# Kernel optimization log

Hardware: AMD Instinct MI355X
Metric: run time of the kernel (lower is better)

Reference implementation:

```python
import math
import jax, jax.numpy as jnp
import numpy as np

B, C, T = 8, 512, 4096
DK = max(C // 8, 2)          # 64
SCALE = math.sqrt(DK)        # 8.0
GAMMA = 1.0                  # source inits gamma=0 (identity); use 1.0 to exercise the attention path
EPS = 1e-12


def _l2_normalize(v):
    return v / (jnp.linalg.norm(v) + EPS)


def setup_inputs() -> dict:
    key = jax.random.key(0)
    ks = jax.random.split(key, 5)
    return {
        "x": jax.random.normal(ks[0], (B, C, T), jnp.float32),
        "Wq": jax.random.normal(ks[1], (DK, C), jnp.float32) * 0.05,
        "Wk": jax.random.normal(ks[2], (DK, C), jnp.float32) * 0.05,
        "Wv": jax.random.normal(ks[3], (C, C), jnp.float32) * 0.05,
        "bv": jnp.zeros((C,), jnp.float32),
        "u": jax.random.normal(ks[4], (C,), jnp.float32),
    }


def reference(x, Wq, Wk, Wv, bv, u):
    # spectral norm on value conv weight (one power iteration, u/v as buffers)
    v = jax.lax.stop_gradient(_l2_normalize(Wv.T @ u))
    u2 = jax.lax.stop_gradient(_l2_normalize(Wv @ v))
    sigma = u2 @ (Wv @ v)
    Wv_sn = Wv / sigma

    # 1x1 conv projections
    q = jnp.einsum('dc,bct->btd', Wq, x)               # [B,T,DK]
    k = jnp.einsum('dc,bct->bdt', Wk, x)               # [B,DK,T]
    energy = jnp.einsum('btd,bds->bts', q, k) / SCALE  # [B,T,T]
    attn = jax.nn.softmax(energy, axis=-1)
    val = jnp.einsum('oc,bct->bot', Wv_sn, x) + bv[None, :, None]  # [B,C,T]
    # out = bmm(value, attention^T): out[b,c,t] = sum_s val[b,c,s]*attn[b,t,s]
    out = jnp.einsum('bcs,bts->bct', val, attn)        # [B,C,T]
    return GAMMA * out + x
```

## Files before the change

### kernel.cpp

```cpp
#include <hip/hip_runtime.h>


#define B_  8
#define C_  512
#define T_  4096
#define DK_ 64

typedef __bf16 bf16x8 __attribute__((ext_vector_type(8)));
typedef float  f32x4  __attribute__((ext_vector_type(4)));

static __device__ __forceinline__ unsigned short f2bf(float f) {
  unsigned u = __float_as_uint(f);
  u += 0x7fffu + ((u >> 16) & 1u);
  return (unsigned short)(u >> 16);
}

#define BAR_LDS() asm volatile("s_waitcnt lgkmcnt(0)\ns_barrier" ::: "memory")

__global__ void sigma_kernel(const float* __restrict__ Wv,
                             const float* __restrict__ u,
                             float* __restrict__ sig) {
  __shared__ float red[512];
  __shared__ float vsh[512];
  __shared__ float snorm;
  int tid = threadIdx.x;

  vsh[tid] = u[tid];
  __syncthreads();
  float acc = 0.f;
  for (int j = 0; j < 512; ++j) acc += Wv[(size_t)j * 512 + tid] * vsh[j];
  red[tid] = acc * acc;
  __syncthreads();
  for (int s = 256; s >= 1; s >>= 1) {
    if (tid < s) red[tid] += red[tid + s];
    __syncthreads();
  }
  if (tid == 0) snorm = sqrtf(red[0]) + 1e-12f;
  __syncthreads();
  float v = acc / snorm;
  __syncthreads();
  vsh[tid] = v;
  __syncthreads();
  float wacc = 0.f;
  for (int c = 0; c < 512; ++c) wacc += Wv[(size_t)tid * 512 + c] * vsh[c];
  red[tid] = wacc * wacc;
  __syncthreads();
  for (int s = 256; s >= 1; s >>= 1) {
    if (tid < s) red[tid] += red[tid + s];
    __syncthreads();
  }
  if (tid == 0) {
    float ww = red[0];
    float sigma = ww / (sqrtf(ww) + 1e-12f);
    sig[0] = 1.f / sigma;
  }
}

__global__ __launch_bounds__(128)
void castw_kernel(const float* __restrict__ Wq, const float* __restrict__ Wk,
                  const float* __restrict__ Wv, const float* __restrict__ sig,
                  unsigned short* __restrict__ Wc) {
  int row = blockIdx.x;
  int c = threadIdx.x * 4;
  const float* src;
  float s;
  if (row < 64) {
    src = Wq + (size_t)row * 512;
    s = 1.4426950408889634f / 8.0f;
  } else if (row < 128) {
    src = Wk + (size_t)(row - 64) * 512;
    s = 1.0f;
  } else {
    src = Wv + (size_t)(row - 128) * 512;
    s = sig[0];
  }
  float4 v = *reinterpret_cast<const float4*>(src + c);
  ushort4 o;
  o.x = f2bf(v.x * s);
  o.y = f2bf(v.y * s);
  o.z = f2bf(v.z * s);
  o.w = f2bf(v.w * s);
  *reinterpret_cast<ushort4*>(Wc + (size_t)row * 512 + c) = o;
}

__global__ __launch_bounds__(256)
void castt_kernel(const float* __restrict__ x, unsigned short* __restrict__ xT) {
  __shared__ __align__(16) unsigned short ldsT[64][72];
  int tid = threadIdx.x;
  int t0 = blockIdx.x * 64, c0 = blockIdx.y * 64, b = blockIdx.z;
  const float* xb = x + ((size_t)b * C_ + c0) * T_ + t0;
#pragma unroll
  for (int k2 = 0; k2 < 4; ++k2) {
    int idx = k2 * 256 + tid;
    int c = idx >> 4, t4 = (idx & 15) * 4;
    float4 v = *reinterpret_cast<const float4*>(xb + (size_t)c * T_ + t4);
    ldsT[t4 + 0][c] = f2bf(v.x);
    ldsT[t4 + 1][c] = f2bf(v.y);
    ldsT[t4 + 2][c] = f2bf(v.z);
    ldsT[t4 + 3][c] = f2bf(v.w);
  }
  __syncthreads();
  unsigned short* xTb = xT + ((size_t)b * T_ + t0) * C_ + c0;
#pragma unroll
  for (int k2 = 0; k2 < 2; ++k2) {
    int idx = k2 * 256 + tid;
    int t = idx >> 3, ch = idx & 7;
    bf16x8 v = *reinterpret_cast<const bf16x8*>(&ldsT[t][ch * 8]);
    *reinterpret_cast<bf16x8*>(xTb + (size_t)t * C_ + ch * 8) = v;
  }
}

__global__ __launch_bounds__(512, 2)
void proj_kernel(const unsigned short* __restrict__ Wc,
                 const unsigned short* __restrict__ xT,
                 const float* __restrict__ bv,
                 unsigned short* __restrict__ Q,
                 unsigned short* __restrict__ Kk,
                 unsigned short* __restrict__ V) {
  __shared__ __align__(16) char smem[98304];
  const int tid = threadIdx.x;
  const int w = tid >> 6;
  const int lane = tid & 63;
  const int col = lane & 15;
  const int g = lane >> 4;
  const int b = blockIdx.x & 7;
  const int t0 = (blockIdx.x >> 3) * 128;

  const unsigned short* xTb = xT + ((size_t)b * T_ + t0) * C_;

  auto stageX = [&](int bsel, int kc) {
    int off = w * 1024 + lane * 16;
    int tl = off >> 6;
    int cb = off & 63;
    const unsigned short* src = xTb + (size_t)tl * C_ + kc + cb / 2;
    __builtin_amdgcn_global_load_lds(
        (const __attribute__((address_space(1))) unsigned int*)src,
        (__attribute__((address_space(3))) unsigned int*)(smem + bsel * 8192 + off),
        16, 0, 0);
  };
  auto stageW = [&](int bsel, int kc) {
#pragma unroll
    for (int i = 0; i < 5; ++i) {
      int off = i * 8192 + w * 1024 + lane * 16;
      int o = off >> 6;
      int cb = off & 63;
      const unsigned short* src = Wc + (size_t)o * 512 + kc + cb / 2;
      __builtin_amdgcn_global_load_lds(
          (const __attribute__((address_space(1))) unsigned int*)src,
          (__attribute__((address_space(3))) unsigned int*)(smem + 16384 + bsel * 40960 + off),
          16, 0, 0);
    }
  };

  f32x4 acc[5][8];
#pragma unroll
  for (int of = 0; of < 5; ++of)
#pragma unroll
    for (int j = 0; j < 8; ++j) acc[of][j] = (f32x4){0.f, 0.f, 0.f, 0.f};

  stageX(0, 0);
  stageW(0, 0);
  __syncthreads();
  int cur = 0;

  for (int ks = 0; ks < 16; ++ks) {
    int kc = ks * 32;
    if (ks < 15) {
      stageX(cur ^ 1, kc + 32);
      stageW(cur ^ 1, kc + 32);
    }
    bf16x8 af[5], bfr[8];
#pragma unroll
    for (int of = 0; of < 5; ++of) {
      int o = w * 80 + of * 16 + col;
      af[of] = *reinterpret_cast<const bf16x8*>(smem + 16384 + cur * 40960 + o * 64 + g * 16);
    }
#pragma unroll
    for (int j = 0; j < 8; ++j) {
      int tl = 16 * j + col;
      bfr[j] = *reinterpret_cast<const bf16x8*>(smem + cur * 8192 + tl * 64 + g * 16);
    }
#pragma unroll
    for (int of = 0; of < 5; ++of)
#pragma unroll
      for (int j = 0; j < 8; ++j)
        acc[of][j] = __builtin_amdgcn_mfma_f32_16x16x32_bf16(af[of], bfr[j], acc[of][j], 0, 0, 0);
    __syncthreads();
    cur ^= 1;
  }

  unsigned short* qkt = (unsigned short*)smem;
  unsigned short* vt = (unsigned short*)(smem + 34816 + w * 4352);
  unsigned short* Vb = V + (size_t)b * C_ * T_;

#pragma unroll
  for (int of = 0; of < 5; ++of) {
    int o0 = w * 80 + of * 16;
    if (o0 < 128) {
#pragma unroll
      for (int j = 0; j < 8; ++j)
#pragma unroll
        for (int r = 0; r < 4; ++r)
          qkt[(16 * j + col) * 136 + o0 + g * 4 + r] = f2bf(acc[of][j][r]);
    } else {
      int c0 = o0 - 128;
      float bvr[4];
#pragma unroll
      for (int r = 0; r < 4; ++r) bvr[r] = bv[c0 + g * 4 + r];
#pragma unroll
      for (int j = 0; j < 8; ++j)
#pragma unroll
        for (int r = 0; r < 4; ++r)
          vt[(g * 4 + r) * 136 + 16 * j + col] = f2bf(acc[of][j][r] + bvr[r]);
#pragma unroll
      for (int p = 0; p < 4; ++p) {
        int o_r = p * 4 + g;
        bf16x8 v8 = *reinterpret_cast<const bf16x8*>((char*)vt + o_r * 272 + col * 16);
        *reinterpret_cast<bf16x8*>(Vb + (size_t)(c0 + o_r) * T_ + t0 + col * 8) = v8;
      }
    }
  }
  __syncthreads();
  unsigned short* Qb = Q + (size_t)b * T_ * DK_;
  unsigned short* Kb = Kk + (size_t)b * T_ * DK_;
#pragma unroll
  for (int k2 = 0; k2 < 2; ++k2) {
    int idx = k2 * 512 + tid;
    int t = idx >> 3, ch = idx & 7;
    bf16x8 q8 = *reinterpret_cast<const bf16x8*>(&qkt[t * 136 + ch * 8]);
    *reinterpret_cast<bf16x8*>(Qb + (size_t)(t0 + t) * DK_ + ch * 8) = q8;
    bf16x8 k8 = *reinterpret_cast<const bf16x8*>(&qkt[t * 136 + 64 + ch * 8]);
    *reinterpret_cast<bf16x8*>(Kb + (size_t)(t0 + t) * DK_ + ch * 8) = k8;
  }
}

__global__ __launch_bounds__(512, 2)
void flash_kernel(const unsigned short* __restrict__ Q,
                  const unsigned short* __restrict__ Kk,
                  const unsigned short* __restrict__ V,
                  const float* __restrict__ x, float* __restrict__ out) {
  __shared__ __align__(16) unsigned short v_lds[2][C_ * 64];
  __shared__ __align__(16) unsigned short p_lds[128 * 64];
  __shared__ __align__(16) float scale_lds[8][16];
  __shared__ __align__(16) float l_lds[128];
  __shared__ unsigned long long flags_lds;

  const int tid = threadIdx.x;
  const int w = tid >> 6;
  const int lane = tid & 63;
  const int col = lane & 15;
  const int g = lane >> 4;
  const int b = blockIdx.x & 7;
  const int t0 = (blockIdx.x >> 3) * 128;
  const int trow0 = t0 + w * 16;

  const unsigned short* Qb = Q + (size_t)b * T_ * DK_;
  const unsigned short* Kb = Kk + (size_t)b * T_ * DK_;
  const unsigned short* Vb = V + (size_t)b * C_ * T_;

  auto stage = [&](int bsel, int s0) {
#pragma unroll
    for (int i = 0; i < 8; ++i) {
      int o = i * 8192 + tid * 16;
      int c = o >> 7;
      int z = (o & 127) ^ ((c & 7) << 4);
      const unsigned short* src = Vb + (size_t)c * T_ + s0 + (z >> 1);
      void* dst = (char*)(&v_lds[bsel][0]) + i * 8192 + w * 1024;
      __builtin_amdgcn_global_load_lds(
          (const __attribute__((address_space(1))) unsigned int*)src,
          (__attribute__((address_space(3))) unsigned int*)dst, 16, 0, 0);
    }
  };

  bf16x8 qf[2];
  {
    const unsigned short* qrow = Qb + (size_t)(trow0 + col) * DK_ + g * 8;
    qf[0] = *reinterpret_cast<const bf16x8*>(qrow);
    qf[1] = *reinterpret_cast<const bf16x8*>(qrow + 32);
  }
  bf16x8 kf[2][4];
  auto loadK = [&](int s0) {
#pragma unroll
    for (int ks = 0; ks < 2; ++ks)
#pragma unroll
      for (int j = 0; j < 4; ++j)
        kf[ks][j] = *reinterpret_cast<const bf16x8*>(
            Kb + (size_t)(s0 + col + 16 * j) * DK_ + 32 * ks + g * 8);
  };

  float m_run = -1e30f, l_run = 0.f;
  f32x4 o_acc[8][4];
#pragma unroll
  for (int qt = 0; qt < 8; ++qt)
#pragma unroll
    for (int ct = 0; ct < 4; ++ct) o_acc[qt][ct] = (f32x4){0.f, 0.f, 0.f, 0.f};

  stage(0, 0);
  loadK(0);
  __syncthreads();
  int cur = 0;

  const float RTHR = 10.0f;
  const int prow = w * 16 + col;
  const int pswz = (prow & 7) << 4;

  for (int it = 0; it < T_ / 64; ++it) {
    f32x4 sacc[4];
#pragma unroll
    for (int j = 0; j < 4; ++j) sacc[j] = (f32x4){0.f, 0.f, 0.f, 0.f};
#pragma unroll
    for (int ks = 0; ks < 2; ++ks)
#pragma unroll
      for (int j = 0; j < 4; ++j)
        sacc[j] = __builtin_amdgcn_mfma_f32_16x16x32_bf16(kf[ks][j], qf[ks], sacc[j], 0, 0, 0);

    float t01 = fmaxf(fmaxf(sacc[0][0], sacc[0][1]), fmaxf(sacc[0][2], sacc[0][3]));
    float t23 = fmaxf(fmaxf(sacc[1][0], sacc[1][1]), fmaxf(sacc[1][2], sacc[1][3]));
    float t45 = fmaxf(fmaxf(sacc[2][0], sacc[2][1]), fmaxf(sacc[2][2], sacc[2][3]));
    float t67 = fmaxf(fmaxf(sacc[3][0], sacc[3][1]), fmaxf(sacc[3][2], sacc[3][3]));
    float tm = fmaxf(fmaxf(t01, t23), fmaxf(t45, t67));
    tm = fmaxf(tm, __shfl_xor(tm, 16));
    tm = fmaxf(tm, __shfl_xor(tm, 32));
    int wave_any = __any(tm > m_run + RTHR);
    float sc = 1.0f;
    if (wave_any) {
      float m_new = fmaxf(m_run, tm);
      sc = exp2f(m_run - m_new);
      m_run = m_new;
      if (lane < 16) scale_lds[w][lane] = sc;
    }
    if (lane == 0)
      ((volatile unsigned char*)&flags_lds)[w] = (unsigned char)wave_any;

    BAR_LDS();

    unsigned long long fl = flags_lds;
    if (fl) {
#pragma unroll
      for (int qt = 0; qt < 8; ++qt) {
        if ((fl >> (8 * qt)) & 0xffull) {
          f32x4 s4 = *reinterpret_cast<const f32x4*>(&scale_lds[qt][4 * g]);
#pragma unroll
          for (int ct = 0; ct < 4; ++ct) o_acc[qt][ct] *= s4;
        }
      }
    }

    float rs = 0.f;
#pragma unroll
    for (int j = 0; j < 4; ++j) {
      float p0 = exp2f(sacc[j][0] - m_run);
      float p1 = exp2f(sacc[j][1] - m_run);
      float p2 = exp2f(sacc[j][2] - m_run);
      float p3 = exp2f(sacc[j][3] - m_run);
      rs += (p0 + p1) + (p2 + p3);
      ushort4 pk = {f2bf(p0), f2bf(p1), f2bf(p2), f2bf(p3)};
      int byteoff = prow * 128 + (((16 * j + 4 * g) * 2) ^ pswz);
      *reinterpret_cast<ushort4*>((char*)p_lds + byteoff) = pk;
    }
    rs += __shfl_xor(rs, 16);
    rs += __shfl_xor(rs, 32);
    l_run = l_run * sc + rs;

    if (it + 1 < T_ / 64) {
      loadK(64 * (it + 1));
      stage(cur ^ 1, 64 * (it + 1));
    }

    BAR_LDS();
    asm volatile("s_waitcnt vmcnt(16)" ::: "memory");

    const char* vbase = (const char*)v_lds[cur];
#pragma unroll
    for (int ks = 0; ks < 2; ++ks) {
      bf16x8 vf[4];
#pragma unroll
      for (int ct = 0; ct < 4; ++ct) {
        int c_ = 64 * w + 16 * ct + col;
        vf[ct] = *reinterpret_cast<const bf16x8*>(
            vbase + c_ * 128 + ((64 * ks + 16 * g) ^ ((c_ & 7) << 4)));
      }
#pragma unroll
      for (int qt = 0; qt < 8; ++qt) {
        int row = 16 * qt + col;
        bf16x8 pa = *reinterpret_cast<const bf16x8*>(
            (const char*)p_lds + row * 128 + ((64 * ks + 16 * g) ^ ((row & 7) << 4)));
#pragma unroll
        for (int ct = 0; ct < 4; ++ct)
          o_acc[qt][ct] = __builtin_amdgcn_mfma_f32_16x16x32_bf16(pa, vf[ct], o_acc[qt][ct], 0, 0, 0);
      }
    }
    cur ^= 1;
  }

  if (lane < 16) l_lds[w * 16 + lane] = l_run;
  BAR_LDS();

  const float* xb = x + (size_t)b * C_ * T_;
  float* ob = out + (size_t)b * C_ * T_;
#pragma unroll
  for (int qt = 0; qt < 8; ++qt) {
    f32x4 l4 = *reinterpret_cast<const f32x4*>(&l_lds[16 * qt + 4 * g]);
    f32x4 linv;
#pragma unroll
    for (int r = 0; r < 4; ++r) linv[r] = 1.f / l4[r];
#pragma unroll
    for (int ct = 0; ct < 4; ++ct) {
      size_t idx = (size_t)(64 * w + 16 * ct + col) * T_ + t0 + 16 * qt + 4 * g;
      f32x4 xv = *reinterpret_cast<const f32x4*>(xb + idx);
      f32x4 o = o_acc[qt][ct];
#pragma unroll
      for (int r = 0; r < 4; ++r) o[r] = o[r] * linv[r] + xv[r];
      *reinterpret_cast<f32x4*>(ob + idx) = o;
    }
  }
}

extern "C" void kernel_launch(void* const* d_in, const int* in_sizes, int n_in,
                              void* d_out, int out_size, void* d_ws, size_t ws_size,
                              hipStream_t stream) {
  const float* x  = (const float*)d_in[0];
  const float* Wq = (const float*)d_in[1];
  const float* Wk = (const float*)d_in[2];
  const float* Wv = (const float*)d_in[3];
  const float* bv = (const float*)d_in[4];
  const float* u  = (const float*)d_in[5];
  float* out = (float*)d_out;

  char* ws = (char*)d_ws;
  float* sig = (float*)ws;
  unsigned short* Q  = (unsigned short*)(ws + 1024);
  unsigned short* Kk = (unsigned short*)(ws + 1024 + (size_t)4 * 1024 * 1024);
  unsigned short* V  = (unsigned short*)(ws + 1024 + (size_t)8 * 1024 * 1024);
  unsigned short* xT = (unsigned short*)(ws + 1024 + (size_t)40 * 1024 * 1024);
  unsigned short* Wc = (unsigned short*)(ws + 1024 + (size_t)72 * 1024 * 1024);

  sigma_kernel<<<1, 512, 0, stream>>>(Wv, u, sig);
  castw_kernel<<<640, 128, 0, stream>>>(Wq, Wk, Wv, sig, Wc);
  castt_kernel<<<dim3(T_ / 64, C_ / 64, B_), 256, 0, stream>>>(x, xT);
  proj_kernel<<<256, 512, 0, stream>>>(Wc, xT, bv, Q, Kk, V);
  flash_kernel<<<256, 512, 0, stream>>>(Q, Kk, V, x, out);
}
```

Baseline: 364.6 us.

## Load V fragments directly to registers and double-buffer P to drop a barrier

Removes the LDS staging of V via global_load_lds and instead has each wave load its own V fragments straight from global memory into registers, prefetched after the PV MFMAs. P and the rescale flags/scales are double-buffered by iteration parity, so one of the two per-iteration barriers goes away and the rescale is applied after the single barrier. It also uses hardware exp2 and packed bf16 conversion instructions, and raises wave priority around the MFMA block. The trade-off is higher register pressure and uncoalesced-ish direct global V loads, where each wave re-reads V with less exposure to latency hiding than the async LDS path.

```diff
diff --git a/kernel.cpp b/kernel.cpp
--- a/kernel.cpp
+++ b/kernel.cpp
@@ -13,6 +13,12 @@
   unsigned u = __float_as_uint(f);
   u += 0x7fffu + ((u >> 16) & 1u);
   return (unsigned short)(u >> 16);
+}
+
+static __device__ __forceinline__ unsigned cvt_pk_bf16(float a, float b) {
+  unsigned r;
+  asm("v_cvt_pk_bf16_f32 %0, %1, %2" : "=v"(r) : "v"(a), "v"(b));
+  return r;
 }
 
 #define BAR_LDS() asm volatile("s_waitcnt lgkmcnt(0)\ns_barrier" ::: "memory")
@@ -239,11 +245,10 @@
                   const unsigned short* __restrict__ Kk,
                   const unsigned short* __restrict__ V,
                   const float* __restrict__ x, float* __restrict__ out) {
-  __shared__ __align__(16) unsigned short v_lds[2][C_ * 64];
-  __shared__ __align__(16) unsigned short p_lds[128 * 64];
-  __shared__ __align__(16) float scale_lds[8][16];
+  __shared__ __align__(16) unsigned short p_lds[2][128 * 64];
+  __shared__ __align__(16) float scale_lds[2][8][16];
   __shared__ __align__(16) float l_lds[128];
-  __shared__ unsigned long long flags_lds;
+  __shared__ unsigned long long flags_lds[2];
 
   const int tid = threadIdx.x;
   const int w = tid >> 6;
@@ -258,26 +263,13 @@
   const unsigned short* Kb = Kk + (size_t)b * T_ * DK_;
   const unsigned short* Vb = V + (size_t)b * C_ * T_;
 
-  auto stage = [&](int bsel, int s0) {
-#pragma unroll
-    for (int i = 0; i < 8; ++i) {
-      int o = i * 8192 + tid * 16;
-      int c = o >> 7;
-      int z = (o & 127) ^ ((c & 7) << 4);
-      const unsigned short* src = Vb + (size_t)c * T_ + s0 + (z >> 1);
-      void* dst = (char*)(&v_lds[bsel][0]) + i * 8192 + w * 1024;
-      __builtin_amdgcn_global_load_lds(
-          (const __attribute__((address_space(1))) unsigned int*)src,
-          (__attribute__((address_space(3))) unsigned int*)dst, 16, 0, 0);
-    }
-  };
-
   bf16x8 qf[2];
   {
     const unsigned short* qrow = Qb + (size_t)(trow0 + col) * DK_ + g * 8;
     qf[0] = *reinterpret_cast<const bf16x8*>(qrow);
     qf[1] = *reinterpret_cast<const bf16x8*>(qrow + 32);
   }
+
   bf16x8 kf[2][4];
   auto loadK = [&](int s0) {
 #pragma unroll
@@ -287,6 +279,15 @@
         kf[ks][j] = *reinterpret_cast<const bf16x8*>(
             Kb + (size_t)(s0 + col + 16 * j) * DK_ + 32 * ks + g * 8);
   };
+  bf16x8 vf[2][4];
+  auto loadV = [&](int s0) {
+#pragma unroll
+    for (int ks = 0; ks < 2; ++ks)
+#pragma unroll
+      for (int ct = 0; ct < 4; ++ct)
+        vf[ks][ct] = *reinterpret_cast<const bf16x8*>(
+            Vb + (size_t)(64 * w + 16 * ct + col) * T_ + s0 + 32 * ks + 8 * g);
+  };
 
   float m_run = -1e30f, l_run = 0.f;
   f32x4 o_acc[8][4];
@@ -295,16 +296,17 @@
 #pragma unroll
     for (int ct = 0; ct < 4; ++ct) o_acc[qt][ct] = (f32x4){0.f, 0.f, 0.f, 0.f};
 
-  stage(0, 0);
   loadK(0);
-  __syncthreads();
-  int cur = 0;
+  loadV(0);
 
   const float RTHR = 10.0f;
   const int prow = w * 16 + col;
   const int pswz = (prow & 7) << 4;
 
   for (int it = 0; it < T_ / 64; ++it) {
+    const int par = it & 1;
+    char* pbase = (char*)p_lds + par * 16384;
+
     f32x4 sacc[4];
 #pragma unroll
     for (int j = 0; j < 4; ++j) sacc[j] = (f32x4){0.f, 0.f, 0.f, 0.f};
@@ -314,83 +316,73 @@
       for (int j = 0; j < 4; ++j)
         sacc[j] = __builtin_amdgcn_mfma_f32_16x16x32_bf16(kf[ks][j], qf[ks], sacc[j], 0, 0, 0);
 
-    float t01 = fmaxf(fmaxf(sacc[0][0], sacc[0][1]), fmaxf(sacc[0][2], sacc[0][3]));
-    float t23 = fmaxf(fmaxf(sacc[1][0], sacc[1][1]), fmaxf(sacc[1][2], sacc[1][3]));
-    float t45 = fmaxf(fmaxf(sacc[2][0], sacc[2][1]), fmaxf(sacc[2][2], sacc[2][3]));
-    float t67 = fmaxf(fmaxf(sacc[3][0], sacc[3][1]), fmaxf(sacc[3][2], sacc[3][3]));
-    float tm = fmaxf(fmaxf(t01, t23), fmaxf(t45, t67));
+    if (it + 1 < T_ / 64) loadK(64 * (it + 1));
+
+    float v0 = fmaxf(fmaxf(sacc[0][0], sacc[0][1]), sacc[0][2]);
+    float v1 = fmaxf(fmaxf(sacc[0][3], sacc[1][0]), sacc[1][1]);
+    float v2 = fmaxf(fmaxf(sacc[1][2], sacc[1][3]), sacc[2][0]);
+    float v3 = fmaxf(fmaxf(sacc[2][1], sacc[2][2]), sacc[2][3]);
+    float v4 = fmaxf(fmaxf(sacc[3][0], sacc[3][1]), sacc[3][2]);
+    float tm = fmaxf(fmaxf(fmaxf(v0, v1), fmaxf(v2, v3)), fmaxf(v4, sacc[3][3]));
     tm = fmaxf(tm, __shfl_xor(tm, 16));
     tm = fmaxf(tm, __shfl_xor(tm, 32));
+
     int wave_any = __any(tm > m_run + RTHR);
     float sc = 1.0f;
     if (wave_any) {
       float m_new = fmaxf(m_run, tm);
-      sc = exp2f(m_run - m_new);
+      sc = __builtin_amdgcn_exp2f(m_run - m_new);
       m_run = m_new;
-      if (lane < 16) scale_lds[w][lane] = sc;
+      if (lane < 16) scale_lds[par][w][lane] = sc;
     }
     if (lane == 0)
-      ((volatile unsigned char*)&flags_lds)[w] = (unsigned char)wave_any;
-
-    BAR_LDS();
-
-    unsigned long long fl = flags_lds;
-    if (fl) {
-#pragma unroll
-      for (int qt = 0; qt < 8; ++qt) {
-        if ((fl >> (8 * qt)) & 0xffull) {
-          f32x4 s4 = *reinterpret_cast<const f32x4*>(&scale_lds[qt][4 * g]);
-#pragma unroll
-          for (int ct = 0; ct < 4; ++ct) o_acc[qt][ct] *= s4;
-        }
-      }
-    }
+      ((volatile unsigned char*)&flags_lds[par])[w] = (unsigned char)wave_any;
 
     float rs = 0.f;
+    char* prow_base = pbase + prow * 128;
 #pragma unroll
     for (int j = 0; j < 4; ++j) {
-      float p0 = exp2f(sacc[j][0] - m_run);
-      float p1 = exp2f(sacc[j][1] - m_run);
-      float p2 = exp2f(sacc[j][2] - m_run);
-      float p3 = exp2f(sacc[j][3] - m_run);
+      float p0 = __builtin_amdgcn_exp2f(sacc[j][0] - m_run);
+      float p1 = __builtin_amdgcn_exp2f(sacc[j][1] - m_run);
+      float p2 = __builtin_amdgcn_exp2f(sacc[j][2] - m_run);
+      float p3 = __builtin_amdgcn_exp2f(sacc[j][3] - m_run);
       rs += (p0 + p1) + (p2 + p3);
-      ushort4 pk = {f2bf(p0), f2bf(p1), f2bf(p2), f2bf(p3)};
-      int byteoff = prow * 128 + (((16 * j + 4 * g) * 2) ^ pswz);
-      *reinterpret_cast<ushort4*>((char*)p_lds + byteoff) = pk;
+      uint2 pk2 = {cvt_pk_bf16(p0, p1), cvt_pk_bf16(p2, p3)};
+      *reinterpret_cast<uint2*>(prow_base + (((16 * j + 4 * g) * 2) ^ pswz)) = pk2;
     }
     rs += __shfl_xor(rs, 16);
     rs += __shfl_xor(rs, 32);
     l_run = l_run * sc + rs;
 
-    if (it + 1 < T_ / 64) {
-      loadK(64 * (it + 1));
-      stage(cur ^ 1, 64 * (it + 1));
-    }
-
     BAR_LDS();
-    asm volatile("s_waitcnt vmcnt(16)" ::: "memory");
-
-    const char* vbase = (const char*)v_lds[cur];
+
+    unsigned long long fl = flags_lds[par];
+    if (fl) {
+#pragma unroll
+      for (int qt = 0; qt < 8; ++qt)
+        if ((fl >> (8 * qt)) & 0xffull) {
+          f32x4 s4 = *reinterpret_cast<const f32x4*>(&scale_lds[par][qt][4 * g]);
+#pragma unroll
+          for (int ct = 0; ct < 4; ++ct) o_acc[qt][ct] *= s4;
+        }
+    }
+
+    __builtin_amdgcn_s_setprio(1);
 #pragma unroll
     for (int ks = 0; ks < 2; ++ks) {
-      bf16x8 vf[4];
-#pragma unroll
-      for (int ct = 0; ct < 4; ++ct) {
-        int c_ = 64 * w + 16 * ct + col;
-        vf[ct] = *reinterpret_cast<const bf16x8*>(
-            vbase + c_ * 128 + ((64 * ks + 16 * g) ^ ((c_ & 7) << 4)));
-      }
 #pragma unroll
       for (int qt = 0; qt < 8; ++qt) {
         int row = 16 * qt + col;
         bf16x8 pa = *reinterpret_cast<const bf16x8*>(
-            (const char*)p_lds + row * 128 + ((64 * ks + 16 * g) ^ ((row & 7) << 4)));
+            pbase + row * 128 + ((64 * ks + 16 * g) ^ ((row & 7) << 4)));
 #pragma unroll
         for (int ct = 0; ct < 4; ++ct)
-          o_acc[qt][ct] = __builtin_amdgcn_mfma_f32_16x16x32_bf16(pa, vf[ct], o_acc[qt][ct], 0, 0, 0);
+          o_acc[qt][ct] = __builtin_amdgcn_mfma_f32_16x16x32_bf16(pa, vf[ks][ct], o_acc[qt][ct], 0, 0, 0);
       }
     }
-    cur ^= 1;
+    __builtin_amdgcn_s_setprio(0);
+
+    if (it + 1 < T_ / 64) loadV(64 * (it + 1));
   }
 
   if (lane < 16) l_lds[w * 16 + lane] = l_run;
```

New measurement: 414.1 us. +13.6%, slower.
